# Optimization experiments

Measured on AMD Instinct MI355X. Metric: run time of the kernel, lower is better.

Reference implementation:

```python
import jax, jax.numpy as jnp
import numpy as np


def _hippo_scale_params(N, L):
    """Replicates HiPPOScale.__init__ for discretization='bilinear' (pure numpy)."""
    q = np.arange(N, dtype=np.float64)
    col, row = np.meshgrid(q, q)
    r = 2 * q + 1
    M = -(np.where(row >= col, r, 0) - np.diag(q))
    T = np.sqrt(np.diag(2 * q + 1))
    A = T @ M @ np.linalg.inv(T)          # (N, N)
    B = np.diag(T)                         # (N,)
    ts = np.arange(1, L + 1, dtype=np.float64)[:, None, None]  # (L,1,1)
    At = A[None] / ts                      # A / t, batched over t
    I = np.eye(N, dtype=np.float64)
    Mm = I[None] - 0.5 * At
    Nn = I[None] + 0.5 * At
    A_stacked = np.linalg.solve(Mm, Nn)                      # (L, N, N)
    Bt = B[None, :] / ts[:, 0, :]                             # (L, N)
    B_stacked = np.linalg.solve(Mm, Bt[..., None])[..., 0]    # (L, N)
    return A_stacked.astype(np.float32), B_stacked.astype(np.float32)


def setup_inputs() -> dict:
    N, L, Bsz = 64, 4096, 64
    key = jax.random.key(0)
    A_st, B_st = _hippo_scale_params(N, L)
    inputs = jax.random.normal(key, (L, Bsz), dtype=jnp.float32)
    return {
        "inputs": inputs,                       # (L, B)
        "A_stacked": jnp.asarray(A_st),         # (L, N, N)
        "B_stacked": jnp.asarray(B_st),         # (L, N)
    }


def reference(inputs, A_stacked, B_stacked):
    # u[t, b, :] = inputs[t, b] * B_stacked[t, :]   -> (L, B, N)
    u = inputs[..., None] * B_stacked[:, None, :]

    # x[t] = A[t] @ x[t-1] + u[t], x[-1] = 0  (time-varying linear recurrence).
    # The torch code computes this via a divide-and-conquer unroll; here we use
    # the equivalent parallel associative scan with elements (A, u) and
    # composition (A2@A1, A2@u1 + u2).
    def combine(e1, e2):
        a1, u1 = e1
        a2, u2 = e2
        a = jnp.matmul(a2, a1)                                  # (l, N, N)
        v = jnp.einsum('...ij,...bj->...bi', a2, u1) + u2       # (l, B, N)
        return (a, v)

    _, x = jax.lax.associative_scan(combine, (A_stacked, u))
    return x  # (L, B, N)
```

## Files before the change

kernel.cpp:

```cpp
#include <hip/hip_runtime.h>
#include <hip/hip_bf16.h>

#define TL 4096
#define NB 64
#define CH 8
#define CN 512
#define AS 72

typedef __attribute__((ext_vector_type(8))) short short8;
typedef __attribute__((ext_vector_type(4))) short short4v;
typedef __attribute__((ext_vector_type(4))) float floatx4;
typedef __attribute__((ext_vector_type(4))) unsigned int uint4v;

__device__ inline floatx4 mfma_bf16(short8 a, short8 b, floatx4 c) {
    return __builtin_amdgcn_mfma_f32_16x16x32_bf16(a, b, c, 0, 0, 0);
}
__device__ inline short bf16_rne(float x) {
    union { __hip_bfloat16 b; unsigned short s; } u;
    u.b = __float2bfloat16(x);
    return (short)u.s;
}
__device__ inline void split_bf16(float x, short& h, short& l) {
    h = bf16_rne(x);
    union { unsigned u; float f; } hv; hv.u = ((unsigned)(unsigned short)h) << 16;
    l = bf16_rne(x - hv.f);
}
__device__ inline void cvt_frag(float4 a, float4 b, short8& H, short8& L) {
    float v[8] = {a.x,a.y,a.z,a.w,b.x,b.y,b.z,b.w};
#pragma unroll
    for (int r = 0; r < 8; ++r) { short hh,ll; split_bf16(v[r],hh,ll); H[r]=hh; L[r]=ll; }
}
__device__ inline void unpack_frag(uint4v a, uint4v b, short8& H, short8& L) {
#pragma unroll
    for (int r = 0; r < 4; ++r) {
        H[r]   = (short)(a[r] >> 16); L[r]   = (short)(a[r] & 0xFFFFu);
        H[4+r] = (short)(b[r] >> 16); L[4+r] = (short)(b[r] & 0xFFFFu);
    }
}

__global__ __launch_bounds__(256, 2)
void hippo_phase1(const float* __restrict__ inp, const float* __restrict__ Ag,
                  const float* __restrict__ Bst,
                  unsigned* __restrict__ P32, float* __restrict__ VT)
{
    __shared__ short SBh[2][NB][AS], SBl[2][NB][AS];
    __shared__ short VBh[2][NB][AS], VBl[2][NB][AS];

    const int tid = threadIdx.x;
    const int c = blockIdx.x, t0 = c * CH;
    const int w = tid >> 6, lane = tid & 63;
    const int quad = lane >> 4, l15 = lane & 15;
    const int arow = 16*w + l15;
    const int wr0  = 16*w + 4*quad;

    float4 rA[2][2];
#pragma unroll
    for (int kc = 0; kc < 2; ++kc) {
        const float* p = Ag + (size_t)(t0+1)*4096 + (size_t)arow*64 + 32*kc + 8*quad;
        rA[kc][0] = *(const float4*)p;
        rA[kc][1] = *(const float4*)(p + 4);
    }
    float4 bnxt = *(const float4*)(Bst + (size_t)(t0+1)*64 + wr0);
    float inxt[4];
#pragma unroll
    for (int ni = 0; ni < 4; ++ni) inxt[ni] = inp[(size_t)(t0+1)*64 + l15 + 16*ni];

    floatx4 accS[4], accV[4];
    {
        const float* A0 = Ag + (size_t)t0 * 4096;
        float4 b0 = *(const float4*)(Bst + (size_t)t0*64 + wr0);
        float bc[4] = {b0.x,b0.y,b0.z,b0.w};
#pragma unroll
        for (int ni = 0; ni < 4; ++ni) {
            const float ii = inp[(size_t)t0*64 + l15 + 16*ni];
#pragma unroll
            for (int r = 0; r < 4; ++r) {
                accS[ni][r] = A0[(size_t)(wr0 + r)*64 + l15 + 16*ni];
                accV[ni][r] = bc[r] * ii;
            }
        }
    }
#pragma unroll
    for (int ni = 0; ni < 4; ++ni) {
        const int cc = l15 + 16*ni;
        short4v h4, l4;
#pragma unroll
        for (int r = 0; r < 4; ++r) { short hh,ll; split_bf16(accS[ni][r],hh,ll); h4[r]=hh; l4[r]=ll; }
        *(short4v*)&SBh[0][cc][wr0] = h4; *(short4v*)&SBl[0][cc][wr0] = l4;
#pragma unroll
        for (int r = 0; r < 4; ++r) { short hh,ll; split_bf16(accV[ni][r],hh,ll); h4[r]=hh; l4[r]=ll; }
        *(short4v*)&VBh[0][cc][wr0] = h4; *(short4v*)&VBl[0][cc][wr0] = l4;
    }
    __syncthreads();

    short8 aH[2], aL[2];
#pragma unroll
    for (int kc = 0; kc < 2; ++kc) cvt_frag(rA[kc][0], rA[kc][1], aH[kc], aL[kc]);

    int cur = 0;
    float4 bcur = bnxt;
    float icur[4];
#pragma unroll
    for (int ni = 0; ni < 4; ++ni) icur[ni] = inxt[ni];

    for (int s = 1; s < CH; ++s) {
        if (s + 1 < CH) {
            const int t1 = t0 + s + 1;
#pragma unroll
            for (int kc = 0; kc < 2; ++kc) {
                const float* p = Ag + (size_t)t1*4096 + (size_t)arow*64 + 32*kc + 8*quad;
                rA[kc][0] = *(const float4*)p;
                rA[kc][1] = *(const float4*)(p + 4);
            }
            bnxt = *(const float4*)(Bst + (size_t)t1*64 + wr0);
#pragma unroll
            for (int ni = 0; ni < 4; ++ni) inxt[ni] = inp[(size_t)t1*64 + l15 + 16*ni];
        }
        {
            float bc[4] = {bcur.x,bcur.y,bcur.z,bcur.w};
#pragma unroll
            for (int ni = 0; ni < 4; ++ni)
#pragma unroll
            for (int r = 0; r < 4; ++r) {
                accS[ni][r] = 0.0f;
                accV[ni][r] = bc[r] * icur[ni];
            }
        }
#pragma unroll
        for (int kc = 0; kc < 2; ++kc) {
            const int ko = 32*kc + 8*quad;
#pragma unroll
            for (int ni = 0; ni < 4; ++ni) {
                const int n = l15 + 16*ni;
                short8 sH = *(const short8*)&SBh[cur][n][ko];
                short8 sL = *(const short8*)&SBl[cur][n][ko];
                short8 vH = *(const short8*)&VBh[cur][n][ko];
                short8 vL = *(const short8*)&VBl[cur][n][ko];
                accS[ni] = mfma_bf16(aH[kc], sH, accS[ni]);
                accS[ni] = mfma_bf16(aH[kc], sL, accS[ni]);
                accS[ni] = mfma_bf16(aL[kc], sH, accS[ni]);
                accV[ni] = mfma_bf16(aH[kc], vH, accV[ni]);
                accV[ni] = mfma_bf16(aH[kc], vL, accV[ni]);
                accV[ni] = mfma_bf16(aL[kc], vH, accV[ni]);
            }
        }
        if (s + 1 < CH) {
#pragma unroll
            for (int kc = 0; kc < 2; ++kc) cvt_frag(rA[kc][0], rA[kc][1], aH[kc], aL[kc]);
            const int nb = cur ^ 1;
#pragma unroll
            for (int ni = 0; ni < 4; ++ni) {
                const int cc = l15 + 16*ni;
                short4v h4, l4;
#pragma unroll
                for (int r = 0; r < 4; ++r) { short hh,ll; split_bf16(accS[ni][r],hh,ll); h4[r]=hh; l4[r]=ll; }
                *(short4v*)&SBh[nb][cc][wr0] = h4; *(short4v*)&SBl[nb][cc][wr0] = l4;
#pragma unroll
                for (int r = 0; r < 4; ++r) { short hh,ll; split_bf16(accV[ni][r],hh,ll); h4[r]=hh; l4[r]=ll; }
                *(short4v*)&VBh[nb][cc][wr0] = h4; *(short4v*)&VBl[nb][cc][wr0] = l4;
            }
            __syncthreads();
            cur ^= 1;
        }
        bcur = bnxt;
#pragma unroll
        for (int ni = 0; ni < 4; ++ni) icur[ni] = inxt[ni];
    }

    unsigned* po = P32 + (size_t)c * 4096;
#pragma unroll
    for (int ni = 0; ni < 4; ++ni) {
        const int cc = l15 + 16*ni;
        *(floatx4*)(VT + (size_t)c*4096 + cc*64 + wr0) = accV[ni];
#pragma unroll
        for (int r = 0; r < 4; ++r) {
            short hh, ll; split_bf16(accS[ni][r], hh, ll);
            po[(size_t)(wr0 + r)*64 + cc] = ((unsigned)(unsigned short)hh << 16) | (unsigned)(unsigned short)ll;
        }
    }
}

__global__ __launch_bounds__(256, 2)
void hippo_scan(unsigned* __restrict__ P32, float* __restrict__ VT,
                unsigned* __restrict__ gbar)
{
    __shared__ short PBh[2][NB][AS], PBl[2][NB][AS];
    __shared__ short VBh[2][NB][AS], VBl[2][NB][AS];

    const int tid = threadIdx.x, c = blockIdx.x;
    const int w = tid >> 6, lane = tid & 63;
    const int quad = lane >> 4, l15 = lane & 15;
    const int arow = 16*w + l15;
    const int wr0  = 16*w + 4*quad;

    auto scan8 = [&](int base, int estride) {
        {
            const unsigned* p0 = P32 + (size_t)base * 4096;
            const float*    v0 = VT  + (size_t)base * 4096;
#pragma unroll
            for (int q = 0; q < 4; ++q) {
                int f = tid + q * 256;
                int k = f & 63, m0 = (f >> 6) * 4;
                uint4v pk = *(const uint4v*)(p0 + k * 64 + m0);
#pragma unroll
                for (int r = 0; r < 4; ++r) {
                    PBh[0][m0 + r][k] = (short)(pk[r] >> 16);
                    PBl[0][m0 + r][k] = (short)(pk[r] & 0xFFFFu);
                }
            }
#pragma unroll
            for (int q = 0; q < 4; ++q) {
                int f = tid + q * 256;
                int n = f >> 4, k0 = (f & 15) * 4;
                float4 vv = *(const float4*)(v0 + n * 64 + k0);
                float va[4] = {vv.x, vv.y, vv.z, vv.w};
                short4v vh4, vl4;
#pragma unroll
                for (int r = 0; r < 4; ++r) { short hh, ll; split_bf16(va[r], hh, ll); vh4[r]=hh; vl4[r]=ll; }
                *(short4v*)&VBh[0][n][k0] = vh4; *(short4v*)&VBl[0][n][k0] = vl4;
            }
        }
        uint4v rP[2][2]; float4 pV[4];
        {
            const unsigned* pc = P32 + (size_t)(base + estride) * 4096;
            const float*    vc = VT  + (size_t)(base + estride) * 4096;
#pragma unroll
            for (int kc = 0; kc < 2; ++kc) {
                const unsigned* p = pc + (size_t)arow*64 + 32*kc + 8*quad;
                rP[kc][0] = *(const uint4v*)p;
                rP[kc][1] = *(const uint4v*)(p + 4);
            }
#pragma unroll
            for (int ni = 0; ni < 4; ++ni)
                pV[ni] = *(const float4*)(vc + (size_t)(l15 + 16*ni)*64 + wr0);
        }
        __syncthreads();

        short8 aH[2], aL[2];
#pragma unroll
        for (int kc = 0; kc < 2; ++kc) unpack_frag(rP[kc][0], rP[kc][1], aH[kc], aL[kc]);

        int cur = 0;
        for (int i = 1; i < 8; ++i) {
            const int idx = base + i * estride;
            floatx4 accP[4], accV[4];
#pragma unroll
            for (int ni = 0; ni < 4; ++ni) {
                accV[ni][0] = pV[ni].x; accV[ni][1] = pV[ni].y;
                accV[ni][2] = pV[ni].z; accV[ni][3] = pV[ni].w;
                accP[ni][0]=accP[ni][1]=accP[ni][2]=accP[ni][3]=0.0f;
            }
            if (i + 1 < 8) {
                const unsigned* pc = P32 + (size_t)(base + (i+1) * estride) * 4096;
                const float*    vc = VT  + (size_t)(base + (i+1) * estride) * 4096;
#pragma unroll
                for (int kc = 0; kc < 2; ++kc) {
                    const unsigned* p = pc + (size_t)arow*64 + 32*kc + 8*quad;
                    rP[kc][0] = *(const uint4v*)p;
                    rP[kc][1] = *(const uint4v*)(p + 4);
                }
#pragma unroll
                for (int ni = 0; ni < 4; ++ni)
                    pV[ni] = *(const float4*)(vc + (size_t)(l15 + 16*ni)*64 + wr0);
            }
#pragma unroll
            for (int kc = 0; kc < 2; ++kc) {
                const int ko = 32*kc + 8*quad;
#pragma unroll
                for (int ni = 0; ni < 4; ++ni) {
                    const int n = l15 + 16*ni;
                    short8 pH = *(const short8*)&PBh[cur][n][ko];
                    short8 pL = *(const short8*)&PBl[cur][n][ko];
                    short8 vH = *(const short8*)&VBh[cur][n][ko];
                    short8 vL = *(const short8*)&VBl[cur][n][ko];
                    accP[ni] = mfma_bf16(aH[kc], pH, accP[ni]);
                    accP[ni] = mfma_bf16(aH[kc], pL, accP[ni]);
                    accP[ni] = mfma_bf16(aL[kc], pH, accP[ni]);
                    accV[ni] = mfma_bf16(aH[kc], vH, accV[ni]);
                    accV[ni] = mfma_bf16(aH[kc], vL, accV[ni]);
                    accV[ni] = mfma_bf16(aL[kc], vH, accV[ni]);
                }
            }
            if (i + 1 < 8) {
#pragma unroll
                for (int kc = 0; kc < 2; ++kc) unpack_frag(rP[kc][0], rP[kc][1], aH[kc], aL[kc]);
            }
            unsigned* po = P32 + (size_t)idx * 4096;
            const int nb = cur ^ 1;
#pragma unroll
            for (int ni = 0; ni < 4; ++ni) {
                const int cc = l15 + 16*ni;
                *(floatx4*)(VT + (size_t)idx*4096 + cc*64 + wr0) = accV[ni];
                short4v h4, l4;
#pragma unroll
                for (int r = 0; r < 4; ++r) {
                    short hh, ll; split_bf16(accP[ni][r], hh, ll);
                    po[(size_t)(wr0+r)*64 + cc] = ((unsigned)(unsigned short)hh << 16) | (unsigned)(unsigned short)ll;
                    h4[r]=hh; l4[r]=ll;
                }
                if (i + 1 < 8) {
                    *(short4v*)&PBh[nb][cc][wr0] = h4; *(short4v*)&PBl[nb][cc][wr0] = l4;
                    short4v vh4, vl4;
#pragma unroll
                    for (int r = 0; r < 4; ++r) { short hh,ll; split_bf16(accV[ni][r],hh,ll); vh4[r]=hh; vl4[r]=ll; }
                    *(short4v*)&VBh[nb][cc][wr0] = vh4; *(short4v*)&VBl[nb][cc][wr0] = vl4;
                }
            }
            if (i + 1 < 8) __syncthreads();
            cur ^= 1;
        }
    };

    scan8(c * 8, 1);

    __syncthreads();
    if (tid == 0)
        __hip_atomic_fetch_add(gbar + 0, 1u, __ATOMIC_RELEASE, __HIP_MEMORY_SCOPE_AGENT);
    if (c >= 8) return;
    if (tid == 0) {
        unsigned v;
        do {
            __builtin_amdgcn_s_sleep(8);
            v = __hip_atomic_load(gbar + 0, __ATOMIC_RELAXED, __HIP_MEMORY_SCOPE_AGENT);
        } while (v < 64u);
        (void)__hip_atomic_load(gbar + 0, __ATOMIC_ACQUIRE, __HIP_MEMORY_SCOPE_AGENT);
    }
    __syncthreads();

    scan8(64 * c + 7, 8);

    __syncthreads();
    if (tid == 0)
        __hip_atomic_fetch_add(gbar + 1, 1u, __ATOMIC_RELEASE, __HIP_MEMORY_SCOPE_AGENT);
    if (c != 0) return;
    if (tid == 0) {
        unsigned v;
        do {
            __builtin_amdgcn_s_sleep(8);
            v = __hip_atomic_load(gbar + 1, __ATOMIC_RELAXED, __HIP_MEMORY_SCOPE_AGENT);
        } while (v < 8u);
        (void)__hip_atomic_load(gbar + 1, __ATOMIC_ACQUIRE, __HIP_MEMORY_SCOPE_AGENT);
    }
    __syncthreads();

    {
#pragma unroll
        for (int q = 0; q < 16; ++q) {
            int f = tid + q * 256; PBh[0][f >> 6][f & 63] = 0; PBl[0][f >> 6][f & 63] = 0;
        }
        uint4v rP[2][2]; float4 pV[4];
        {
            const unsigned* pc = P32 + (size_t)63 * 4096;
            const float*    vc = VT  + (size_t)63 * 4096;
#pragma unroll
            for (int kc = 0; kc < 2; ++kc) {
                const unsigned* p = pc + (size_t)arow*64 + 32*kc + 8*quad;
                rP[kc][0] = *(const uint4v*)p;
                rP[kc][1] = *(const uint4v*)(p + 4);
            }
#pragma unroll
            for (int ni = 0; ni < 4; ++ni)
                pV[ni] = *(const float4*)(vc + (size_t)(l15 + 16*ni)*64 + wr0);
        }
        __syncthreads();

        short8 aH[2], aL[2];
#pragma unroll
        for (int kc = 0; kc < 2; ++kc) unpack_frag(rP[kc][0], rP[kc][1], aH[kc], aL[kc]);

        int cur = 0;
        for (int s = 0; s < 7; ++s) {
            const int idx = 64 * s + 63;
            floatx4 acc[4];
#pragma unroll
            for (int ni = 0; ni < 4; ++ni) {
                acc[ni][0] = pV[ni].x; acc[ni][1] = pV[ni].y;
                acc[ni][2] = pV[ni].z; acc[ni][3] = pV[ni].w;
            }
            if (s + 1 < 7) {
                const int idx2 = 64 * (s + 1) + 63;
                const unsigned* pc = P32 + (size_t)idx2 * 4096;
                const float*    vc = VT  + (size_t)idx2 * 4096;
#pragma unroll
                for (int kc = 0; kc < 2; ++kc) {
                    const unsigned* p = pc + (size_t)arow*64 + 32*kc + 8*quad;
                    rP[kc][0] = *(const uint4v*)p;
                    rP[kc][1] = *(const uint4v*)(p + 4);
                }
#pragma unroll
                for (int ni = 0; ni < 4; ++ni)
                    pV[ni] = *(const float4*)(vc + (size_t)(l15 + 16*ni)*64 + wr0);
            }
#pragma unroll
            for (int kc = 0; kc < 2; ++kc) {
                const int ko = 32*kc + 8*quad;
#pragma unroll
                for (int ni = 0; ni < 4; ++ni) {
                    const int n = l15 + 16*ni;
                    short8 eH = *(const short8*)&PBh[cur][n][ko];
                    short8 eL = *(const short8*)&PBl[cur][n][ko];
                    acc[ni] = mfma_bf16(aH[kc], eH, acc[ni]);
                    acc[ni] = mfma_bf16(aH[kc], eL, acc[ni]);
                    acc[ni] = mfma_bf16(aL[kc], eH, acc[ni]);
                }
            }
            if (s + 1 < 7) {
#pragma unroll
                for (int kc = 0; kc < 2; ++kc) unpack_frag(rP[kc][0], rP[kc][1], aH[kc], aL[kc]);
            }
            float* eo = (float*)(P32 + (size_t)idx * 4096);
            const int nb = cur ^ 1;
#pragma unroll
            for (int ni = 0; ni < 4; ++ni) {
                const int cc = l15 + 16*ni;
                *(floatx4*)(eo + cc*64 + wr0) = acc[ni];
                if (s + 1 < 7) {
                    short4v h4, l4;
#pragma unroll
                    for (int r = 0; r < 4; ++r) { short hh,ll; split_bf16(acc[ni][r],hh,ll); h4[r]=hh; l4[r]=ll; }
                    *(short4v*)&PBh[nb][cc][wr0] = h4; *(short4v*)&PBl[nb][cc][wr0] = l4;
                }
            }
            if (s + 1 < 7) __syncthreads();
            cur ^= 1;
        }
    }
}

__global__ __launch_bounds__(256, 2)
void hippo_phase3(const float* __restrict__ inp, const float* __restrict__ Ag,
                  const float* __restrict__ Bst, const unsigned* __restrict__ P32,
                  const float* __restrict__ VT, float* __restrict__ out)
{
    __shared__ short XBh[2][NB][AS], XBl[2][NB][AS];

    const int tid = threadIdx.x, c = blockIdx.x, t0 = c * CH;
    const int w = tid >> 6, lane = tid & 63, quad = lane >> 4, l15 = lane & 15;
    const int arow = 16*w + l15;
    const int wr0  = 16*w + 4*quad;
    const int sup = c >> 6, g = c >> 3, gi = g & 7, j = c & 7;

    float4 rA[2][2];
#pragma unroll
    for (int kc = 0; kc < 2; ++kc) {
        const float* p = Ag + (size_t)t0*4096 + (size_t)arow*64 + 32*kc + 8*quad;
        rA[kc][0] = *(const float4*)p;
        rA[kc][1] = *(const float4*)(p + 4);
    }
    float4 bcur = *(const float4*)(Bst + (size_t)t0*64 + wr0);
    float icur[4];
#pragma unroll
    for (int ni = 0; ni < 4; ++ni) icur[ni] = inp[(size_t)t0*64 + l15 + 16*ni];

    if (sup == 0) {
#pragma unroll
        for (int q = 0; q < 16; ++q) { int f = tid + q*256; XBh[0][f>>6][f&63] = 0; XBl[0][f>>6][f&63] = 0; }
    } else {
        const float* e = (const float*)(P32 + (size_t)(64*(sup-1) + 63) * 4096);
#pragma unroll
        for (int q = 0; q < 4; ++q) {
            int f = tid + q*256; int b = f>>4, k0 = (f&15)*4;
            float4 v = *(const float4*)(e + b*64 + k0);
            float va[4] = {v.x,v.y,v.z,v.w};
            short4v h4, l4;
#pragma unroll
            for (int r=0;r<4;++r){short hh,ll;split_bf16(va[r],hh,ll);h4[r]=hh;l4[r]=ll;}
            *(short4v*)&XBh[0][b][k0] = h4; *(short4v*)&XBl[0][b][k0] = l4;
        }
    }
    __syncthreads();
    int cur = 0;

    auto combine = [&](int idx) {
        uint4v rP[2][2];
        const unsigned* pc = P32 + (size_t)idx * 4096;
        const float*    vc = VT  + (size_t)idx * 4096;
#pragma unroll
        for (int kc = 0; kc < 2; ++kc) {
            const unsigned* p = pc + (size_t)arow*64 + 32*kc + 8*quad;
            rP[kc][0] = *(const uint4v*)p;
            rP[kc][1] = *(const uint4v*)(p + 4);
        }
        floatx4 acc[4];
#pragma unroll
        for (int ni = 0; ni < 4; ++ni) {
            float4 vv = *(const float4*)(vc + (size_t)(l15 + 16*ni)*64 + wr0);
            acc[ni][0]=vv.x; acc[ni][1]=vv.y; acc[ni][2]=vv.z; acc[ni][3]=vv.w;
        }
        short8 cH[2], cL[2];
#pragma unroll
        for (int kc = 0; kc < 2; ++kc) unpack_frag(rP[kc][0], rP[kc][1], cH[kc], cL[kc]);
#pragma unroll
        for (int kc = 0; kc < 2; ++kc) {
            const int ko = 32*kc + 8*quad;
#pragma unroll
            for (int ni = 0; ni < 4; ++ni) {
                const int n = l15 + 16*ni;
                short8 xH = *(const short8*)&XBh[cur][n][ko];
                short8 xL = *(const short8*)&XBl[cur][n][ko];
                acc[ni] = mfma_bf16(cH[kc], xH, acc[ni]);
                acc[ni] = mfma_bf16(cH[kc], xL, acc[ni]);
                acc[ni] = mfma_bf16(cL[kc], xH, acc[ni]);
            }
        }
        const int nb = cur ^ 1;
#pragma unroll
        for (int ni = 0; ni < 4; ++ni) {
            const int cc = l15 + 16*ni;
            short4v h4, l4;
#pragma unroll
            for (int r=0;r<4;++r){short hh,ll;split_bf16(acc[ni][r],hh,ll);h4[r]=hh;l4[r]=ll;}
            *(short4v*)&XBh[nb][cc][wr0] = h4; *(short4v*)&XBl[nb][cc][wr0] = l4;
        }
        __syncthreads();
        cur ^= 1;
    };
    if (gi) combine(8*g - 1);
    if (j)  combine(c - 1);

    short8 aH[2], aL[2];
#pragma unroll
    for (int kc = 0; kc < 2; ++kc) cvt_frag(rA[kc][0], rA[kc][1], aH[kc], aL[kc]);

    float4 bnxt; float inxt[4];
    floatx4 acc[4];
    for (int s = 0; s < CH; ++s) {
        const int t = t0 + s;
        if (s + 1 < CH) {
            const int t1 = t + 1;
#pragma unroll
            for (int kc = 0; kc < 2; ++kc) {
                const float* p = Ag + (size_t)t1*4096 + (size_t)arow*64 + 32*kc + 8*quad;
                rA[kc][0] = *(const float4*)p;
                rA[kc][1] = *(const float4*)(p + 4);
            }
            bnxt = *(const float4*)(Bst + (size_t)t1*64 + wr0);
#pragma unroll
            for (int ni = 0; ni < 4; ++ni) inxt[ni] = inp[(size_t)t1*64 + l15 + 16*ni];
        }
        {
            float bc[4] = {bcur.x,bcur.y,bcur.z,bcur.w};
#pragma unroll
            for (int ni=0;ni<4;++ni)
#pragma unroll
            for (int r=0;r<4;++r) acc[ni][r] = bc[r] * icur[ni];
        }
#pragma unroll
        for (int kc = 0; kc < 2; ++kc) {
            const int ko = 32*kc + 8*quad;
#pragma unroll
            for (int ni = 0; ni < 4; ++ni) {
                const int n = l15 + 16*ni;
                short8 xH = *(const short8*)&XBh[cur][n][ko];
                short8 xL = *(const short8*)&XBl[cur][n][ko];
                acc[ni] = mfma_bf16(aH[kc], xH, acc[ni]);
                acc[ni] = mfma_bf16(aH[kc], xL, acc[ni]);
                acc[ni] = mfma_bf16(aL[kc], xH, acc[ni]);
            }
        }
        if (s + 1 < CH) {
#pragma unroll
            for (int kc = 0; kc < 2; ++kc) cvt_frag(rA[kc][0], rA[kc][1], aH[kc], aL[kc]);
        }
        const int nb = cur ^ 1;
#pragma unroll
        for (int ni = 0; ni < 4; ++ni) {
            const int cc = l15 + 16*ni;
            *(floatx4*)(out + (size_t)t*4096 + cc*64 + wr0) = acc[ni];
            if (s + 1 < CH) {
                short4v h4, l4;
#pragma unroll
                for (int r=0;r<4;++r){short hh,ll;split_bf16(acc[ni][r],hh,ll);h4[r]=hh;l4[r]=ll;}
                *(short4v*)&XBh[nb][cc][wr0] = h4; *(short4v*)&XBl[nb][cc][wr0] = l4;
            }
        }
        if (s + 1 < CH) { __syncthreads(); cur ^= 1; }
        bcur = bnxt;
#pragma unroll
        for (int ni = 0; ni < 4; ++ni) icur[ni] = inxt[ni];
    }
}

extern "C" void kernel_launch(void* const* d_in, const int* in_sizes, int n_in,
                              void* d_out, int out_size, void* d_ws, size_t ws_size,
                              hipStream_t stream)
{
    const float* inp = (const float*)d_in[0];
    const float* A   = (const float*)d_in[1];
    const float* Bst = (const float*)d_in[2];
    float* out = (float*)d_out;
    float* ws  = (float*)d_ws;

    unsigned* P32 = (unsigned*)ws;
    float*    VT  = (float*)ws + (size_t)CN * 4096;
    unsigned* gbar = (unsigned*)((char*)d_ws + (size_t)16 * 1024 * 1024);

    hipMemsetAsync(gbar, 0, 2 * sizeof(unsigned), stream);
    hippo_phase1<<<CN, 256, 0, stream>>>(inp, A, Bst, P32, VT);
    hippo_scan<<<64, 256, 0, stream>>>(P32, VT, gbar);
    hippo_phase3<<<CN, 256, 0, stream>>>(inp, A, Bst, P32, VT, out);
}
```

Before: 187.6 us.

## Fuse chunk scan into phase1 using last-arriver atomic counters

Merges the separate scan kernel into phase1. Each block increments a per-group atomic counter after writing its chunk summary, and only the last arriving block of each group of 8 goes on to run the level-1 scan, then the level-2 scan, then the final carry scan. This removes a kernel launch and the spin-wait barriers, and lets the scan overlap with other phase1 blocks still working. The scan now runs inside the heavier phase1 blocks, and correctness depends on acquire/release ordering of the atomics.

Result: slower. 224.5 us (+19.7%).

```diff
diff --git a/kernel.cpp b/kernel.cpp
--- a/kernel.cpp
+++ b/kernel.cpp
@@ -41,10 +41,12 @@
 __global__ __launch_bounds__(256, 2)
 void hippo_phase1(const float* __restrict__ inp, const float* __restrict__ Ag,
                   const float* __restrict__ Bst,
-                  unsigned* __restrict__ P32, float* __restrict__ VT)
+                  unsigned* __restrict__ P32, float* __restrict__ VT,
+                  unsigned* __restrict__ gbar)
 {
     __shared__ short SBh[2][NB][AS], SBl[2][NB][AS];
     __shared__ short VBh[2][NB][AS], VBl[2][NB][AS];
+    __shared__ unsigned who;
 
     const int tid = threadIdx.x;
     const int c = blockIdx.x, t0 = c * CH;
@@ -167,31 +169,19 @@
         for (int ni = 0; ni < 4; ++ni) icur[ni] = inxt[ni];
     }
 
-    unsigned* po = P32 + (size_t)c * 4096;
-#pragma unroll
-    for (int ni = 0; ni < 4; ++ni) {
-        const int cc = l15 + 16*ni;
-        *(floatx4*)(VT + (size_t)c*4096 + cc*64 + wr0) = accV[ni];
-#pragma unroll
-        for (int r = 0; r < 4; ++r) {
-            short hh, ll; split_bf16(accS[ni][r], hh, ll);
-            po[(size_t)(wr0 + r)*64 + cc] = ((unsigned)(unsigned short)hh << 16) | (unsigned)(unsigned short)ll;
-        }
-    }
-}
-
-__global__ __launch_bounds__(256, 2)
-void hippo_scan(unsigned* __restrict__ P32, float* __restrict__ VT,
-                unsigned* __restrict__ gbar)
-{
-    __shared__ short PBh[2][NB][AS], PBl[2][NB][AS];
-    __shared__ short VBh[2][NB][AS], VBl[2][NB][AS];
-
-    const int tid = threadIdx.x, c = blockIdx.x;
-    const int w = tid >> 6, lane = tid & 63;
-    const int quad = lane >> 4, l15 = lane & 15;
-    const int arow = 16*w + l15;
-    const int wr0  = 16*w + 4*quad;
+    {
+        unsigned* po = P32 + (size_t)c * 4096;
+#pragma unroll
+        for (int ni = 0; ni < 4; ++ni) {
+            const int cc = l15 + 16*ni;
+            *(floatx4*)(VT + (size_t)c*4096 + cc*64 + wr0) = accV[ni];
+#pragma unroll
+            for (int r = 0; r < 4; ++r) {
+                short hh, ll; split_bf16(accS[ni][r], hh, ll);
+                po[(size_t)(wr0 + r)*64 + cc] = ((unsigned)(unsigned short)hh << 16) | (unsigned)(unsigned short)ll;
+            }
+        }
+    }
 
     auto scan8 = [&](int base, int estride) {
         {
@@ -204,8 +194,8 @@
                 uint4v pk = *(const uint4v*)(p0 + k * 64 + m0);
 #pragma unroll
                 for (int r = 0; r < 4; ++r) {
-                    PBh[0][m0 + r][k] = (short)(pk[r] >> 16);
-                    PBl[0][m0 + r][k] = (short)(pk[r] & 0xFFFFu);
+                    SBh[0][m0 + r][k] = (short)(pk[r] >> 16);
+                    SBl[0][m0 + r][k] = (short)(pk[r] & 0xFFFFu);
                 }
             }
 #pragma unroll
@@ -236,19 +226,19 @@
         }
         __syncthreads();
 
-        short8 aH[2], aL[2];
-#pragma unroll
-        for (int kc = 0; kc < 2; ++kc) unpack_frag(rP[kc][0], rP[kc][1], aH[kc], aL[kc]);
-
-        int cur = 0;
+        short8 sH2[2], sL2[2];
+#pragma unroll
+        for (int kc = 0; kc < 2; ++kc) unpack_frag(rP[kc][0], rP[kc][1], sH2[kc], sL2[kc]);
+
+        int cb = 0;
         for (int i = 1; i < 8; ++i) {
             const int idx = base + i * estride;
-            floatx4 accP[4], accV[4];
-#pragma unroll
-            for (int ni = 0; ni < 4; ++ni) {
-                accV[ni][0] = pV[ni].x; accV[ni][1] = pV[ni].y;
-                accV[ni][2] = pV[ni].z; accV[ni][3] = pV[ni].w;
-                accP[ni][0]=accP[ni][1]=accP[ni][2]=accP[ni][3]=0.0f;
+            floatx4 accP2[4], accV2[4];
+#pragma unroll
+            for (int ni = 0; ni < 4; ++ni) {
+                accV2[ni][0] = pV[ni].x; accV2[ni][1] = pV[ni].y;
+                accV2[ni][2] = pV[ni].z; accV2[ni][3] = pV[ni].w;
+                accP2[ni][0]=accP2[ni][1]=accP2[ni][2]=accP2[ni][3]=0.0f;
             }
             if (i + 1 < 8) {
                 const unsigned* pc = P32 + (size_t)(base + (i+1) * estride) * 4096;
@@ -269,84 +259,76 @@
 #pragma unroll
                 for (int ni = 0; ni < 4; ++ni) {
                     const int n = l15 + 16*ni;
-                    short8 pH = *(const short8*)&PBh[cur][n][ko];
-                    short8 pL = *(const short8*)&PBl[cur][n][ko];
-                    short8 vH = *(const short8*)&VBh[cur][n][ko];
-                    short8 vL = *(const short8*)&VBl[cur][n][ko];
-                    accP[ni] = mfma_bf16(aH[kc], pH, accP[ni]);
-                    accP[ni] = mfma_bf16(aH[kc], pL, accP[ni]);
-                    accP[ni] = mfma_bf16(aL[kc], pH, accP[ni]);
-                    accV[ni] = mfma_bf16(aH[kc], vH, accV[ni]);
-                    accV[ni] = mfma_bf16(aH[kc], vL, accV[ni]);
-                    accV[ni] = mfma_bf16(aL[kc], vH, accV[ni]);
+                    short8 pH = *(const short8*)&SBh[cb][n][ko];
+                    short8 pL = *(const short8*)&SBl[cb][n][ko];
+                    short8 vH = *(const short8*)&VBh[cb][n][ko];
+                    short8 vL = *(const short8*)&VBl[cb][n][ko];
+                    accP2[ni] = mfma_bf16(sH2[kc], pH, accP2[ni]);
+                    accP2[ni] = mfma_bf16(sH2[kc], pL, accP2[ni]);
+                    accP2[ni] = mfma_bf16(sL2[kc], pH, accP2[ni]);
+                    accV2[ni] = mfma_bf16(sH2[kc], vH, accV2[ni]);
+                    accV2[ni] = mfma_bf16(sH2[kc], vL, accV2[ni]);
+                    accV2[ni] = mfma_bf16(sL2[kc], vH, accV2[ni]);
                 }
             }
             if (i + 1 < 8) {
 #pragma unroll
-                for (int kc = 0; kc < 2; ++kc) unpack_frag(rP[kc][0], rP[kc][1], aH[kc], aL[kc]);
+                for (int kc = 0; kc < 2; ++kc) unpack_frag(rP[kc][0], rP[kc][1], sH2[kc], sL2[kc]);
             }
             unsigned* po = P32 + (size_t)idx * 4096;
-            const int nb = cur ^ 1;
+            const int nb = cb ^ 1;
 #pragma unroll
             for (int ni = 0; ni < 4; ++ni) {
                 const int cc = l15 + 16*ni;
-                *(floatx4*)(VT + (size_t)idx*4096 + cc*64 + wr0) = accV[ni];
+                *(floatx4*)(VT + (size_t)idx*4096 + cc*64 + wr0) = accV2[ni];
                 short4v h4, l4;
 #pragma unroll
                 for (int r = 0; r < 4; ++r) {
-                    short hh, ll; split_bf16(accP[ni][r], hh, ll);
+                    short hh, ll; split_bf16(accP2[ni][r], hh, ll);
                     po[(size_t)(wr0+r)*64 + cc] = ((unsigned)(unsigned short)hh << 16) | (unsigned)(unsigned short)ll;
                     h4[r]=hh; l4[r]=ll;
                 }
                 if (i + 1 < 8) {
-                    *(short4v*)&PBh[nb][cc][wr0] = h4; *(short4v*)&PBl[nb][cc][wr0] = l4;
+                    *(short4v*)&SBh[nb][cc][wr0] = h4; *(short4v*)&SBl[nb][cc][wr0] = l4;
                     short4v vh4, vl4;
 #pragma unroll
-                    for (int r = 0; r < 4; ++r) { short hh,ll; split_bf16(accV[ni][r],hh,ll); vh4[r]=hh; vl4[r]=ll; }
+                    for (int r = 0; r < 4; ++r) { short hh,ll; split_bf16(accV2[ni][r],hh,ll); vh4[r]=hh; vl4[r]=ll; }
                     *(short4v*)&VBh[nb][cc][wr0] = vh4; *(short4v*)&VBl[nb][cc][wr0] = vl4;
                 }
             }
             if (i + 1 < 8) __syncthreads();
-            cur ^= 1;
+            cb ^= 1;
         }
     };
 
-    scan8(c * 8, 1);
-
+    const int g = c >> 3;
     __syncthreads();
     if (tid == 0)
-        __hip_atomic_fetch_add(gbar + 0, 1u, __ATOMIC_RELEASE, __HIP_MEMORY_SCOPE_AGENT);
-    if (c >= 8) return;
-    if (tid == 0) {
-        unsigned v;
-        do {
-            __builtin_amdgcn_s_sleep(8);
-            v = __hip_atomic_load(gbar + 0, __ATOMIC_RELAXED, __HIP_MEMORY_SCOPE_AGENT);
-        } while (v < 64u);
-        (void)__hip_atomic_load(gbar + 0, __ATOMIC_ACQUIRE, __HIP_MEMORY_SCOPE_AGENT);
-    }
-    __syncthreads();
-
-    scan8(64 * c + 7, 8);
-
+        who = __hip_atomic_fetch_add(gbar + g, 1u, __ATOMIC_ACQ_REL, __HIP_MEMORY_SCOPE_AGENT);
+    __syncthreads();
+    if (who != 7u) return;
+
+    scan8(g * 8, 1);
+
+    const int sp = g >> 3;
     __syncthreads();
     if (tid == 0)
-        __hip_atomic_fetch_add(gbar + 1, 1u, __ATOMIC_RELEASE, __HIP_MEMORY_SCOPE_AGENT);
-    if (c != 0) return;
-    if (tid == 0) {
-        unsigned v;
-        do {
-            __builtin_amdgcn_s_sleep(8);
-            v = __hip_atomic_load(gbar + 1, __ATOMIC_RELAXED, __HIP_MEMORY_SCOPE_AGENT);
-        } while (v < 8u);
-        (void)__hip_atomic_load(gbar + 1, __ATOMIC_ACQUIRE, __HIP_MEMORY_SCOPE_AGENT);
-    }
-    __syncthreads();
+        who = __hip_atomic_fetch_add(gbar + 64 + sp, 1u, __ATOMIC_ACQ_REL, __HIP_MEMORY_SCOPE_AGENT);
+    __syncthreads();
+    if (who != 7u) return;
+
+    scan8(64 * sp + 7, 8);
+
+    __syncthreads();
+    if (tid == 0)
+        who = __hip_atomic_fetch_add(gbar + 72, 1u, __ATOMIC_ACQ_REL, __HIP_MEMORY_SCOPE_AGENT);
+    __syncthreads();
+    if (who != 7u) return;
 
     {
 #pragma unroll
         for (int q = 0; q < 16; ++q) {
-            int f = tid + q * 256; PBh[0][f >> 6][f & 63] = 0; PBl[0][f >> 6][f & 63] = 0;
+            int f = tid + q * 256; SBh[0][f >> 6][f & 63] = 0; SBl[0][f >> 6][f & 63] = 0;
         }
         uint4v rP[2][2]; float4 pV[4];
         {
@@ -364,11 +346,11 @@
         }
         __syncthreads();
 
-        short8 aH[2], aL[2];
-#pragma unroll
-        for (int kc = 0; kc < 2; ++kc) unpack_frag(rP[kc][0], rP[kc][1], aH[kc], aL[kc]);
-
-        int cur = 0;
+        short8 eAH[2], eAL[2];
+#pragma unroll
+        for (int kc = 0; kc < 2; ++kc) unpack_frag(rP[kc][0], rP[kc][1], eAH[kc], eAL[kc]);
+
+        int cb = 0;
         for (int s = 0; s < 7; ++s) {
             const int idx = 64 * s + 63;
             floatx4 acc[4];
@@ -397,19 +379,19 @@
 #pragma unroll
                 for (int ni = 0; ni < 4; ++ni) {
                     const int n = l15 + 16*ni;
-                    short8 eH = *(const short8*)&PBh[cur][n][ko];
-                    short8 eL = *(const short8*)&PBl[cur][n][ko];
-                    acc[ni] = mfma_bf16(aH[kc], eH, acc[ni]);
-                    acc[ni] = mfma_bf16(aH[kc], eL, acc[ni]);
-                    acc[ni] = mfma_bf16(aL[kc], eH, acc[ni]);
+                    short8 eH = *(const short8*)&SBh[cb][n][ko];
+                    short8 eL = *(const short8*)&SBl[cb][n][ko];
+                    acc[ni] = mfma_bf16(eAH[kc], eH, acc[ni]);
+                    acc[ni] = mfma_bf16(eAH[kc], eL, acc[ni]);
+                    acc[ni] = mfma_bf16(eAL[kc], eH, acc[ni]);
                 }
             }
             if (s + 1 < 7) {
 #pragma unroll
-                for (int kc = 0; kc < 2; ++kc) unpack_frag(rP[kc][0], rP[kc][1], aH[kc], aL[kc]);
+                for (int kc = 0; kc < 2; ++kc) unpack_frag(rP[kc][0], rP[kc][1], eAH[kc], eAL[kc]);
             }
             float* eo = (float*)(P32 + (size_t)idx * 4096);
-            const int nb = cur ^ 1;
+            const int nb = cb ^ 1;
 #pragma unroll
             for (int ni = 0; ni < 4; ++ni) {
                 const int cc = l15 + 16*ni;
@@ -418,11 +400,11 @@
                     short4v h4, l4;
 #pragma unroll
                     for (int r = 0; r < 4; ++r) { short hh,ll; split_bf16(acc[ni][r],hh,ll); h4[r]=hh; l4[r]=ll; }
-                    *(short4v*)&PBh[nb][cc][wr0] = h4; *(short4v*)&PBl[nb][cc][wr0] = l4;
+                    *(short4v*)&SBh[nb][cc][wr0] = h4; *(short4v*)&SBl[nb][cc][wr0] = l4;
                 }
             }
             if (s + 1 < 7) __syncthreads();
-            cur ^= 1;
+            cb ^= 1;
         }
     }
 }
@@ -595,8 +577,7 @@
     float*    VT  = (float*)ws + (size_t)CN * 4096;
     unsigned* gbar = (unsigned*)((char*)d_ws + (size_t)16 * 1024 * 1024);
 
-    hipMemsetAsync(gbar, 0, 2 * sizeof(unsigned), stream);
-    hippo_phase1<<<CN, 256, 0, stream>>>(inp, A, Bst, P32, VT);
-    hippo_scan<<<64, 256, 0, stream>>>(P32, VT, gbar);
+    hipMemsetAsync(gbar, 0, 128 * sizeof(unsigned), stream);
+    hippo_phase1<<<CN, 256, 0, stream>>>(inp, A, Bst, P32, VT, gbar);
     hippo_phase3<<<CN, 256, 0, stream>>>(inp, A, Bst, P32, VT, out);
 }
```
